# Optimization experiments

Measured on AMD Instinct MI355X. Metric: run time of the kernel, lower is better.

The kernel has to match this reference:

```python
import jax, jax.numpy as jnp
import numpy as np

B, T, D, H, HS = 4, 1024, 1024, 16, 64
DW, DA, DG, DV = 64, 64, 128, 32
DM = H * HS  # == D here
EPS = 1e-5
DECAY_C = -0.606531  # -exp(-0.5)


def setup_inputs() -> dict:
    key = jax.random.key(0)
    ks = jax.random.split(key, 24)
    n = lambda k, s: jax.random.normal(k, s, dtype=jnp.float32)
    w = lambda k, s: n(k, s) * (1.0 / np.sqrt(s[0]))
    return dict(
        current=n(ks[0], (B, T, D)),
        prev=n(ks[1], (B, T, D)),
        v_first=n(ks[2], (B, T, DM)),
        rwkvag=jax.random.uniform(ks[3], (6, D), dtype=jnp.float32),
        rw_W=w(ks[4], (D, D)),
        w1=w(ks[5], (D, DW)), w2=w(ks[6], (DW, DM)), w2_b=n(ks[7], (DM,)) * 0.1,
        kw_W=w(ks[8], (D, DM)), vw_W=w(ks[9], (D, DM)),
        a1=w(ks[10], (D, DA)), a2=w(ks[11], (DA, DM)), a2_b=n(ks[12], (DM,)) * 0.1,
        v1=w(ks[13], (D, DV)), v2=w(ks[14], (DV, DM)), v2_b=n(ks[15], (DM,)) * 0.1,
        g1=w(ks[16], (D, DG)), g2=w(ks[17], (DG, DM)), g2_b=n(ks[18], (DM,)) * 0.1,
        k_k=jnp.ones((DM,)), k_a=jax.random.uniform(ks[19], (DM,), dtype=jnp.float32),
        r_k=jnp.ones((DM,)),
        gn_scale=jnp.ones((DM,)), gn_bias=jnp.zeros((DM,)),
        out_W=w(ks[20], (DM, D)),
    )


def _add_heads(x):
    return x.reshape(x.shape[:-1] + (H, HS))


def reference(current, prev, v_first, rwkvag, rw_W, w1, w2, w2_b, kw_W, vw_W,
              a1, a2, a2_b, v1, v2, v2_b, g1, g2, g2_b,
              k_k, k_a, r_k, gn_scale, gn_bias, out_W):
    diff = prev - current
    # per-channel token-shift mixing for the 6 branches: (B,T,6,D)
    x6 = current[..., None, :] + rwkvag * diff[..., None, :]
    xr, xw, xk, xv, xa, xg = (x6[..., i, :] for i in range(6))

    r = xr @ rw_W
    wl = jnp.tanh(xw @ w1) @ w2 + w2_b          # w-LoRA (tanh, bias_post)
    k = xk @ kw_W
    v = xv @ vw_W
    a = jax.nn.sigmoid((xa @ a1) @ a2 + a2_b)   # a-LoRA (bias_post) + sigmoid
    g = jax.nn.sigmoid(xg @ g1) @ g2 + g2_b     # g-LoRA (sigmoid act)

    kk = _add_heads(k * k_k)
    kk = kk / jnp.linalg.norm(kk, axis=-1, keepdims=True)
    k = k * (1.0 + (a - 1.0) * k_a)
    v = v + (v_first - v) * jax.nn.sigmoid((xv @ v1) @ v2 + v2_b)
    wdec = jnp.exp(DECAY_C * jax.nn.sigmoid(wl))  # decay in (exp(-0.6065), 1)

    rk_sum = _add_heads(r * k * r_k).sum(-1, keepdims=True)  # (B,T,H,1)
    rh, wh, kh, vh = _add_heads(r), _add_heads(wdec), _add_heads(k), _add_heads(v)
    at = -kk
    bt = kk * _add_heads(a)

    def step(state, xs):
        rt, wt, ktt, vt, att, btt = xs  # each (B,H,HS)
        sa = jnp.einsum('bhvk,bhk->bhv', state, att)
        state = (state * wt[:, :, None, :]
                 + sa[..., None] * btt[:, :, None, :]
                 + vt[..., None] * ktt[:, :, None, :])
        y = jnp.einsum('bhvk,bhk->bhv', state, rt)
        return state, y

    xs = tuple(jnp.moveaxis(x, 1, 0) for x in (rh, wh, kh, vh, at, bt))
    state0 = jnp.zeros((B, H, HS, HS), dtype=current.dtype)
    state, ys = jax.lax.scan(step, state0, xs)
    out = jnp.moveaxis(ys, 0, 1)  # (B,T,H,HS)

    # GroupNorm with n_head groups (normalize within each head)
    mu = out.mean(-1, keepdims=True)
    var = out.var(-1, keepdims=True)
    outn = (out - mu) * jax.lax.rsqrt(var + EPS)
    outn = outn.reshape(B, T, DM) * gn_scale + gn_bias

    outn = outn + (rk_sum * vh).reshape(B, T, DM)
    y = (outn * g) @ out_W
    return y, state, v_first
```

## Files before the change

kernel.cpp:

```cpp
#include <hip/hip_runtime.h>
#include <math.h>

#define NT 4096
#define DD 1024
#define NH 16
#define HSZ 64
#define GN_EPS 1e-5f
#define DECAY_C -0.606531f

typedef __attribute__((ext_vector_type(8))) short short8;
typedef __attribute__((ext_vector_type(4))) float float4v;

#define GLB(p) ((const __attribute__((address_space(1))) void*)(p))
#define LDS(p) ((__attribute__((address_space(3))) void*)(p))

__device__ __forceinline__ float sigm(float x) { return 1.f / (1.f + __expf(-x)); }

__device__ __forceinline__ unsigned short f2bf(float f) {
    unsigned int u = __float_as_uint(f);
    u = (u + 0x7fffu + ((u >> 16) & 1u)) >> 16;
    return (unsigned short)u;
}
__device__ __forceinline__ float bf2f(unsigned short h) {
    return __uint_as_float(((unsigned int)h) << 16);
}

__device__ __forceinline__ float row_sum16(float x) {
    int t;
    t = __builtin_amdgcn_update_dpp(0, __float_as_int(x), 0x128, 0xF, 0xF, true);
    x += __int_as_float(t);
    t = __builtin_amdgcn_update_dpp(0, __float_as_int(x), 0x124, 0xF, 0xF, true);
    x += __int_as_float(t);
    t = __builtin_amdgcn_update_dpp(0, __float_as_int(x), 0x122, 0xF, 0xF, true);
    x += __int_as_float(t);
    t = __builtin_amdgcn_update_dpp(0, __float_as_int(x), 0x121, 0xF, 0xF, true);
    x += __int_as_float(t);
    return x;
}

__global__ __launch_bounds__(256)
void mix6(const float* __restrict__ cur, const float* __restrict__ prev,
          const float* __restrict__ lam,
          ushort* __restrict__ xrh, ushort* __restrict__ xrl,
          ushort* __restrict__ xwh, ushort* __restrict__ xwl,
          ushort* __restrict__ xkh, ushort* __restrict__ xkl,
          ushort* __restrict__ xvh, ushort* __restrict__ xvl,
          ushort* __restrict__ xah, ushort* __restrict__ xal,
          ushort* __restrict__ xgh, ushort* __restrict__ xgl)
{
    const int tok = blockIdx.x;
    const int d0 = threadIdx.x * 4;
    const size_t base = (size_t)tok * DD + d0;
    float4 c = *(const float4*)(cur + base);
    float4 p = *(const float4*)(prev + base);
    float dx = p.x - c.x, dy = p.y - c.y, dz = p.z - c.z, dw = p.w - c.w;
    ushort* hs[6] = {xrh, xwh, xkh, xvh, xah, xgh};
    ushort* ls[6] = {xrl, xwl, xkl, xvl, xal, xgl};
#pragma unroll
    for (int j = 0; j < 6; j++) {
        float4 l = *(const float4*)(lam + j * DD + d0);
        float m0 = c.x + l.x * dx;
        float m1 = c.y + l.y * dy;
        float m2 = c.z + l.z * dz;
        float m3 = c.w + l.w * dw;
        ushort4 h;
        h.x = f2bf(m0); h.y = f2bf(m1); h.z = f2bf(m2); h.w = f2bf(m3);
        *(ushort4*)(hs[j] + base) = h;
        ushort4 lo;
        lo.x = f2bf(m0 - bf2f(h.x));
        lo.y = f2bf(m1 - bf2f(h.y));
        lo.z = f2bf(m2 - bf2f(h.z));
        lo.w = f2bf(m3 - bf2f(h.w));
        *(ushort4*)(ls[j] + base) = lo;
    }
}

__global__ __launch_bounds__(256)
void transpose_pad(const float* __restrict__ W, ushort* __restrict__ Wh,
                   ushort* __restrict__ Wl, int K, int N)
{
    __shared__ float tile[32][33];
    const int bx = blockIdx.x * 32;
    const int by = blockIdx.y * 32;
    const int tx = threadIdx.x, ty = threadIdx.y;
#pragma unroll
    for (int i = 0; i < 32; i += 8) {
        float v = 0.f;
        if (bx + tx < N) v = W[(size_t)(by + ty + i) * N + bx + tx];
        tile[ty + i][tx] = v;
    }
    __syncthreads();
#pragma unroll
    for (int i = 0; i < 32; i += 8) {
        float v = tile[tx][ty + i];
        ushort h = f2bf(v);
        size_t o = (size_t)(bx + ty + i) * K + by + tx;
        Wh[o] = h;
        if (Wl) Wl[o] = f2bf(v - bf2f(h));
    }
}

__global__ __launch_bounds__(256)
void gemm_mega1(const ushort* __restrict__ xrh, const ushort* __restrict__ xrl,
                const ushort* __restrict__ xwh, const ushort* __restrict__ xwl,
                const ushort* __restrict__ xkh, const ushort* __restrict__ xkl,
                const ushort* __restrict__ xvh, const ushort* __restrict__ xvl,
                const ushort* __restrict__ xah, const ushort* __restrict__ xal,
                const ushort* __restrict__ xgh, const ushort* __restrict__ xgl,
                const ushort* __restrict__ Bth, const ushort* __restrict__ Btl,
                float* __restrict__ r_buf, float* __restrict__ k_buf,
                float* __restrict__ v_buf,
                ushort* __restrict__ hwh, ushort* __restrict__ hwl,
                ushort* __restrict__ hah, ushort* __restrict__ hal,
                ushort* __restrict__ hvh, ushort* __restrict__ hvl,
                ushort* __restrict__ hgh, ushort* __restrict__ hgl)
{
    __shared__ ushort AsH[128 * 32];
    __shared__ ushort BsH[128 * 32];
    __shared__ ushort AsL[128 * 32];
    __shared__ ushort BsL[128 * 32];
    const int cb = blockIdx.y;
    const ushort* Ah; const ushort* Al;
    if (cb < 8)       { Ah = xrh; Al = xrl; }
    else if (cb < 16) { Ah = xkh; Al = xkl; }
    else if (cb < 24) { Ah = xvh; Al = xvl; }
    else if (cb == 24){ Ah = xwh; Al = xwl; }
    else if (cb == 25){ Ah = xah; Al = xal; }
    else if (cb == 26){ Ah = xvh; Al = xvl; }
    else              { Ah = xgh; Al = xgl; }

    const int tid = threadIdx.x;
    const int rowBase = blockIdx.x * 128;
    const int colBase = cb * 128;
    const int lane = tid & 63;
    const int wave = tid >> 6;
    const int wm = wave >> 1, wn = wave & 1;
    const int m15 = lane & 15, quad = lane >> 4;

    float4v zero4 = {0.f, 0.f, 0.f, 0.f};
    float4v acc[4][4];
#pragma unroll
    for (int i = 0; i < 4; i++)
#pragma unroll
        for (int j = 0; j < 4; j++) acc[i][j] = zero4;

    for (int k0 = 0; k0 < 1024; k0 += 32) {
#pragma unroll
        for (int i = 0; i < 2; i++) {
            int idx = i * 256 + tid;
            int r = idx >> 2, seg = idx & 3;
            size_t aoff = (size_t)(rowBase + r) * 1024 + k0 + seg * 8;
            size_t boff = (size_t)(colBase + r) * 1024 + k0 + seg * 8;
            int dst = (i * 256 + (tid & ~63)) * 8;
            __builtin_amdgcn_global_load_lds(GLB(Ah + aoff), LDS(AsH + dst), 16, 0, 0);
            __builtin_amdgcn_global_load_lds(GLB(Bth + boff), LDS(BsH + dst), 16, 0, 0);
            __builtin_amdgcn_global_load_lds(GLB(Al + aoff), LDS(AsL + dst), 16, 0, 0);
            __builtin_amdgcn_global_load_lds(GLB(Btl + boff), LDS(BsL + dst), 16, 0, 0);
        }
        __syncthreads();
        short8 ah[4], bh[4], al[4], bl[4];
#pragma unroll
        for (int mi = 0; mi < 4; mi++) {
            ah[mi] = *(const short8*)(AsH + (wm * 64 + mi * 16 + m15) * 32 + quad * 8);
            al[mi] = *(const short8*)(AsL + (wm * 64 + mi * 16 + m15) * 32 + quad * 8);
        }
#pragma unroll
        for (int ni = 0; ni < 4; ni++) {
            bh[ni] = *(const short8*)(BsH + (wn * 64 + ni * 16 + m15) * 32 + quad * 8);
            bl[ni] = *(const short8*)(BsL + (wn * 64 + ni * 16 + m15) * 32 + quad * 8);
        }
#pragma unroll
        for (int mi = 0; mi < 4; mi++)
#pragma unroll
            for (int ni = 0; ni < 4; ni++) {
                acc[mi][ni] = __builtin_amdgcn_mfma_f32_16x16x32_bf16(al[mi], bh[ni], acc[mi][ni], 0, 0, 0);
                acc[mi][ni] = __builtin_amdgcn_mfma_f32_16x16x32_bf16(ah[mi], bl[ni], acc[mi][ni], 0, 0, 0);
                acc[mi][ni] = __builtin_amdgcn_mfma_f32_16x16x32_bf16(ah[mi], bh[ni], acc[mi][ni], 0, 0, 0);
            }
        __syncthreads();
    }

#pragma unroll
    for (int mi = 0; mi < 4; mi++) {
#pragma unroll
        for (int ni = 0; ni < 4; ni++) {
            int c = wn * 64 + ni * 16 + m15;
#pragma unroll
            for (int rr = 0; rr < 4; rr++) {
                int row = rowBase + wm * 64 + mi * 16 + quad * 4 + rr;
                float v = acc[mi][ni][rr];
                if (cb < 24) {
                    float* dst = (cb < 8) ? r_buf : (cb < 16) ? k_buf : v_buf;
                    int n = (cb & 7) * 128 + c;
                    dst[(size_t)row * 1024 + n] = v;
                } else if (cb == 24) {
                    if (c < 64) {
                        float t = tanhf(v);
                        ushort h = f2bf(t);
                        hwh[(size_t)row * 64 + c] = h;
                        hwl[(size_t)row * 64 + c] = f2bf(t - bf2f(h));
                    }
                } else if (cb == 25) {
                    if (c < 64) {
                        ushort h = f2bf(v);
                        hah[(size_t)row * 64 + c] = h;
                        hal[(size_t)row * 64 + c] = f2bf(v - bf2f(h));
                    }
                } else if (cb == 26) {
                    if (c < 32) {
                        ushort h = f2bf(v);
                        hvh[(size_t)row * 32 + c] = h;
                        hvl[(size_t)row * 32 + c] = f2bf(v - bf2f(h));
                    }
                } else {
                    float t = sigm(v);
                    ushort h = f2bf(t);
                    hgh[(size_t)row * 128 + c] = h;
                    hgl[(size_t)row * 128 + c] = f2bf(t - bf2f(h));
                }
            }
        }
    }
}

__global__ __launch_bounds__(256)
void gemm_mega2(const ushort* __restrict__ hwh, const ushort* __restrict__ hwl,
                const ushort* __restrict__ hah, const ushort* __restrict__ hal,
                const ushort* __restrict__ hvh, const ushort* __restrict__ hvl,
                const ushort* __restrict__ hgh, const ushort* __restrict__ hgl,
                const ushort* __restrict__ w2Th, const ushort* __restrict__ w2Tl,
                const ushort* __restrict__ a2Th, const ushort* __restrict__ a2Tl,
                const ushort* __restrict__ v2Th, const ushort* __restrict__ v2Tl,
                const ushort* __restrict__ g2Th, const ushort* __restrict__ g2Tl,
                const float* __restrict__ w2_b, const float* __restrict__ a2_b,
                const float* __restrict__ v2_b, const float* __restrict__ g2_b,
                float* __restrict__ w_buf, float* __restrict__ a_buf,
                float* __restrict__ vg_buf, float* __restrict__ g_buf)
{
    __shared__ ushort AsH[128 * 32];
    __shared__ ushort BsH[128 * 32];
    __shared__ ushort AsL[128 * 32];
    __shared__ ushort BsL[128 * 32];
    const int cb = blockIdx.y;
    const int seg = cb >> 3;
    const int K = (seg == 2) ? 32 : (seg == 3) ? 128 : 64;
    const ushort *Ah, *Al, *Bh, *Bl;
    const float* bias;
    float* outp;
    if (seg == 0) { Ah = hwh; Al = hwl; Bh = w2Th; Bl = w2Tl; bias = w2_b; outp = w_buf; }
    else if (seg == 1) { Ah = hah; Al = hal; Bh = a2Th; Bl = a2Tl; bias = a2_b; outp = a_buf; }
    else if (seg == 2) { Ah = hvh; Al = hvl; Bh = v2Th; Bl = v2Tl; bias = v2_b; outp = vg_buf; }
    else { Ah = hgh; Al = hgl; Bh = g2Th; Bl = g2Tl; bias = g2_b; outp = g_buf; }

    const int tid = threadIdx.x;
    const int rowBase = blockIdx.x * 128;
    const int colBase = (cb & 7) * 128;
    const int lane = tid & 63;
    const int wave = tid >> 6;
    const int wm = wave >> 1, wn = wave & 1;
    const int m15 = lane & 15, quad = lane >> 4;

    float4v zero4 = {0.f, 0.f, 0.f, 0.f};
    float4v acc[4][4];
#pragma unroll
    for (int i = 0; i < 4; i++)
#pragma unroll
        for (int j = 0; j < 4; j++) acc[i][j] = zero4;

    for (int k0 = 0; k0 < K; k0 += 32) {
#pragma unroll
        for (int i = 0; i < 2; i++) {
            int idx = i * 256 + tid;
            int r = idx >> 2, s8 = idx & 3;
            size_t aoff = (size_t)(rowBase + r) * K + k0 + s8 * 8;
            size_t boff = (size_t)(colBase + r) * K + k0 + s8 * 8;
            int dst = (i * 256 + (tid & ~63)) * 8;
            __builtin_amdgcn_global_load_lds(GLB(Ah + aoff), LDS(AsH + dst), 16, 0, 0);
            __builtin_amdgcn_global_load_lds(GLB(Bh + boff), LDS(BsH + dst), 16, 0, 0);
            __builtin_amdgcn_global_load_lds(GLB(Al + aoff), LDS(AsL + dst), 16, 0, 0);
            __builtin_amdgcn_global_load_lds(GLB(Bl + boff), LDS(BsL + dst), 16, 0, 0);
        }
        __syncthreads();
        short8 ah[4], bh[4], al[4], bl[4];
#pragma unroll
        for (int mi = 0; mi < 4; mi++) {
            ah[mi] = *(const short8*)(AsH + (wm * 64 + mi * 16 + m15) * 32 + quad * 8);
            al[mi] = *(const short8*)(AsL + (wm * 64 + mi * 16 + m15) * 32 + quad * 8);
        }
#pragma unroll
        for (int ni = 0; ni < 4; ni++) {
            bh[ni] = *(const short8*)(BsH + (wn * 64 + ni * 16 + m15) * 32 + quad * 8);
            bl[ni] = *(const short8*)(BsL + (wn * 64 + ni * 16 + m15) * 32 + quad * 8);
        }
#pragma unroll
        for (int mi = 0; mi < 4; mi++)
#pragma unroll
            for (int ni = 0; ni < 4; ni++) {
                acc[mi][ni] = __builtin_amdgcn_mfma_f32_16x16x32_bf16(al[mi], bh[ni], acc[mi][ni], 0, 0, 0);
                acc[mi][ni] = __builtin_amdgcn_mfma_f32_16x16x32_bf16(ah[mi], bl[ni], acc[mi][ni], 0, 0, 0);
                acc[mi][ni] = __builtin_amdgcn_mfma_f32_16x16x32_bf16(ah[mi], bh[ni], acc[mi][ni], 0, 0, 0);
            }
        __syncthreads();
    }

#pragma unroll
    for (int mi = 0; mi < 4; mi++) {
#pragma unroll
        for (int ni = 0; ni < 4; ni++) {
            int col = colBase + wn * 64 + ni * 16 + m15;
            float bv = bias[col];
#pragma unroll
            for (int rr = 0; rr < 4; rr++) {
                int row = rowBase + wm * 64 + mi * 16 + quad * 4 + rr;
                float v = acc[mi][ni][rr] + bv;
                if (seg == 1 || seg == 2) v = sigm(v);
                outp[(size_t)row * 1024 + col] = v;
            }
        }
    }
}

__global__ __launch_bounds__(256)
void gemm_bf16s(const ushort* __restrict__ Ah, const ushort* __restrict__ Bh,
                float* __restrict__ outF, int N, int K)
{
    __shared__ ushort AsH[128 * 32];
    __shared__ ushort BsH[128 * 32];
    const int tid = threadIdx.x;
    const int rowBase = blockIdx.x * 128;
    const int colBase = blockIdx.y * 128;
    const int lane = tid & 63;
    const int wave = tid >> 6;
    const int wm = wave >> 1, wn = wave & 1;
    const int m15 = lane & 15, quad = lane >> 4;

    float4v zero4 = {0.f, 0.f, 0.f, 0.f};
    float4v acc[4][4];
#pragma unroll
    for (int i = 0; i < 4; i++)
#pragma unroll
        for (int j = 0; j < 4; j++) acc[i][j] = zero4;

    for (int k0 = 0; k0 < K; k0 += 32) {
#pragma unroll
        for (int i = 0; i < 2; i++) {
            int idx = i * 256 + tid;
            int r = idx >> 2, seg = idx & 3;
            size_t aoff = (size_t)(rowBase + r) * K + k0 + seg * 8;
            size_t boff = (size_t)(colBase + r) * K + k0 + seg * 8;
            int dst = (i * 256 + (tid & ~63)) * 8;
            __builtin_amdgcn_global_load_lds(GLB(Ah + aoff), LDS(AsH + dst), 16, 0, 0);
            __builtin_amdgcn_global_load_lds(GLB(Bh + boff), LDS(BsH + dst), 16, 0, 0);
        }
        __syncthreads();
        short8 ah[4], bh[4];
#pragma unroll
        for (int mi = 0; mi < 4; mi++)
            ah[mi] = *(const short8*)(AsH + (wm * 64 + mi * 16 + m15) * 32 + quad * 8);
#pragma unroll
        for (int ni = 0; ni < 4; ni++)
            bh[ni] = *(const short8*)(BsH + (wn * 64 + ni * 16 + m15) * 32 + quad * 8);
#pragma unroll
        for (int mi = 0; mi < 4; mi++)
#pragma unroll
            for (int ni = 0; ni < 4; ni++)
                acc[mi][ni] = __builtin_amdgcn_mfma_f32_16x16x32_bf16(ah[mi], bh[ni], acc[mi][ni], 0, 0, 0);
        __syncthreads();
    }

#pragma unroll
    for (int mi = 0; mi < 4; mi++) {
#pragma unroll
        for (int ni = 0; ni < 4; ni++) {
            int col = colBase + wn * 64 + ni * 16 + m15;
#pragma unroll
            for (int rr = 0; rr < 4; rr++) {
                int row = rowBase + wm * 64 + mi * 16 + quad * 4 + rr;
                outF[(size_t)row * N + col] = acc[mi][ni][rr];
            }
        }
    }
}

__global__ __launch_bounds__(256)
void elemwise1(const float* __restrict__ r_buf, float* __restrict__ wl_buf,
               float* __restrict__ k_buf, float* __restrict__ v_buf,
               float* __restrict__ kkn_buf, const float* __restrict__ a_buf,
               const float* __restrict__ vg_buf, const float* __restrict__ vfirst,
               const float* __restrict__ kkw, const float* __restrict__ kaw,
               const float* __restrict__ rkw, float* __restrict__ rk_sum)
{
    const int tok = blockIdx.x;
    const int tid = threadIdx.x;
    const int d0 = tid * 4;
    const size_t base = (size_t)tok * DD + d0;

    float4 k0 = *(const float4*)(k_buf + base);
    float4 a4 = *(const float4*)(a_buf + base);
    float4 wl = *(const float4*)(wl_buf + base);
    float4 v0 = *(const float4*)(v_buf + base);
    float4 vg = *(const float4*)(vg_buf + base);
    float4 vf = *(const float4*)(vfirst + base);
    float4 r4 = *(const float4*)(r_buf + base);
    float4 kkc = *(const float4*)(kkw + d0);
    float4 kac = *(const float4*)(kaw + d0);
    float4 rkc = *(const float4*)(rkw + d0);

    float kk0 = k0.x * kkc.x, kk1 = k0.y * kkc.y, kk2 = k0.z * kkc.z, kk3 = k0.w * kkc.w;
    float ss = kk0 * kk0 + kk1 * kk1 + kk2 * kk2 + kk3 * kk3;
    ss += __shfl_xor(ss, 1); ss += __shfl_xor(ss, 2);
    ss += __shfl_xor(ss, 4); ss += __shfl_xor(ss, 8);
    float rn = rsqrtf(ss);
    float4 kkn = { kk0 * rn, kk1 * rn, kk2 * rn, kk3 * rn };
    *(float4*)(kkn_buf + base) = kkn;

    float4 kf;
    kf.x = k0.x * (1.f + (a4.x - 1.f) * kac.x);
    kf.y = k0.y * (1.f + (a4.y - 1.f) * kac.y);
    kf.z = k0.z * (1.f + (a4.z - 1.f) * kac.z);
    kf.w = k0.w * (1.f + (a4.w - 1.f) * kac.w);
    *(float4*)(k_buf + base) = kf;

    float rk = r4.x * kf.x * rkc.x + r4.y * kf.y * rkc.y + r4.z * kf.z * rkc.z + r4.w * kf.w * rkc.w;
    rk += __shfl_xor(rk, 1); rk += __shfl_xor(rk, 2);
    rk += __shfl_xor(rk, 4); rk += __shfl_xor(rk, 8);
    if ((tid & 15) == 0) rk_sum[(size_t)tok * NH + (tid >> 4)] = rk;

    float4 vfin;
    vfin.x = v0.x + (vf.x - v0.x) * vg.x;
    vfin.y = v0.y + (vf.y - v0.y) * vg.y;
    vfin.z = v0.z + (vf.z - v0.z) * vg.z;
    vfin.w = v0.w + (vf.w - v0.w) * vg.w;
    *(float4*)(v_buf + base) = vfin;

    float4 wd;
    wd.x = __expf(DECAY_C * sigm(wl.x));
    wd.y = __expf(DECAY_C * sigm(wl.y));
    wd.z = __expf(DECAY_C * sigm(wl.z));
    wd.w = __expf(DECAY_C * sigm(wl.w));
    *(float4*)(wl_buf + base) = wd;
}

__global__ __launch_bounds__(256)
void scan_kernel(const float* __restrict__ r_buf, const float* __restrict__ w_buf,
                 const float* __restrict__ k_buf, const float* __restrict__ kkn_buf,
                 const float* __restrict__ a_buf, const float* __restrict__ v_buf,
                 float* __restrict__ out_scan, float* __restrict__ state_out)
{
    __shared__ float vec[16][5][64];
    __shared__ float vbuf[16][16];
    __shared__ float ybuf[16][16];
    const int bh = blockIdx.x;
    const int rg = blockIdx.y;
    const int b = bh >> 4, h = bh & 15;
    const int tid = threadIdx.x;
    const int row = tid >> 4, l16 = tid & 15;
    const int rowbase = rg * 16;
    const size_t tok0 = ((size_t)b * 1024) * DD + h * HSZ;
    float s0 = 0.f, s1 = 0.f, s2 = 0.f, s3 = 0.f;

    const int tld = tid >> 4;
    const int lld = (tid & 15) * 4;
    const int ft = tid >> 2, fl = (tid & 3) * 4;

    for (int c = 0; c < 64; c++) {
        if (c > 0 && tid < 64) {
            float4 yv = *(float4*)&ybuf[ft][fl];
            *(float4*)(out_scan + tok0 + (size_t)((c - 1) * 16 + ft) * DD + rowbase + fl) = yv;
        }
#pragma unroll
        for (int j = 0; j < 5; j++) {
            const float* bs = (j == 0) ? r_buf : (j == 1) ? w_buf : (j == 2) ? k_buf
                              : (j == 3) ? kkn_buf : a_buf;
            *(float4*)&vec[tld][j][lld] =
                *(const float4*)(bs + tok0 + (size_t)(c * 16 + tld) * DD + lld);
        }
        if (tid < 64) {
            *(float4*)&vbuf[ft][fl] =
                *(const float4*)(v_buf + tok0 + (size_t)(c * 16 + ft) * DD + rowbase + fl);
        }
        __syncthreads();

        for (int t = 0; t < 16; t++) {
            const float* vp = &vec[t][0][0];
            float4 r4 = *(const float4*)(vp + l16 * 4);
            float4 w4 = *(const float4*)(vp + 64 + l16 * 4);
            float4 k4 = *(const float4*)(vp + 128 + l16 * 4);
            float4 q4 = *(const float4*)(vp + 192 + l16 * 4);
            float4 a4 = *(const float4*)(vp + 256 + l16 * 4);
            float vv = vbuf[t][row];

            float sa = s0 * q4.x + s1 * q4.y + s2 * q4.z + s3 * q4.w;
            sa = row_sum16(sa);
            sa = -sa;

            s0 = s0 * w4.x + sa * (q4.x * a4.x) + vv * k4.x;
            s1 = s1 * w4.y + sa * (q4.y * a4.y) + vv * k4.y;
            s2 = s2 * w4.z + sa * (q4.z * a4.z) + vv * k4.z;
            s3 = s3 * w4.w + sa * (q4.w * a4.w) + vv * k4.w;

            float y = s0 * r4.x + s1 * r4.y + s2 * r4.z + s3 * r4.w;
            y = row_sum16(y);
            if (l16 == 0) ybuf[t][row] = y;
        }
        __syncthreads();
    }

    if (tid < 64) {
        float4 yv = *(float4*)&ybuf[ft][fl];
        *(float4*)(out_scan + tok0 + (size_t)(1008 + ft) * DD + rowbase + fl) = yv;
    }

    float* so = state_out + ((size_t)(b * NH + h) * HSZ + rowbase + row) * HSZ + l16 * 4;
    float4 sv = {s0, s1, s2, s3};
    *(float4*)so = sv;
}

__global__ __launch_bounds__(256)
void elemwise2(const float* __restrict__ out_scan, const float* __restrict__ rk_sum,
               const float* __restrict__ v_buf, const float* __restrict__ g_buf,
               const float* __restrict__ gscale, const float* __restrict__ gbias,
               ushort* __restrict__ z_buf)
{
    const int tok = blockIdx.x;
    const int tid = threadIdx.x;
    const int d0 = tid * 4;
    const size_t base = (size_t)tok * DD + d0;

    float4 o = *(const float4*)(out_scan + base);
    float sm = o.x + o.y + o.z + o.w;
    float ss = o.x * o.x + o.y * o.y + o.z * o.z + o.w * o.w;
    sm += __shfl_xor(sm, 1); sm += __shfl_xor(sm, 2);
    sm += __shfl_xor(sm, 4); sm += __shfl_xor(sm, 8);
    ss += __shfl_xor(ss, 1); ss += __shfl_xor(ss, 2);
    ss += __shfl_xor(ss, 4); ss += __shfl_xor(ss, 8);
    float mu = sm * (1.f / 64.f);
    float var = ss * (1.f / 64.f) - mu * mu;
    float rs = rsqrtf(var + GN_EPS);
    float rk = rk_sum[(size_t)tok * NH + (tid >> 4)];

    float4 v4 = *(const float4*)(v_buf + base);
    float4 g4 = *(const float4*)(g_buf + base);
    float4 gs = *(const float4*)(gscale + d0);
    float4 gb = *(const float4*)(gbias + d0);
    ushort4 z;
    z.x = f2bf(((o.x - mu) * rs * gs.x + gb.x + rk * v4.x) * g4.x);
    z.y = f2bf(((o.y - mu) * rs * gs.y + gb.y + rk * v4.y) * g4.y);
    z.z = f2bf(((o.z - mu) * rs * gs.z + gb.z + rk * v4.z) * g4.z);
    z.w = f2bf(((o.w - mu) * rs * gs.w + gb.w + rk * v4.w) * g4.w);
    *(ushort4*)(z_buf + base) = z;
}

extern "C" void kernel_launch(void* const* d_in, const int* in_sizes, int n_in,
                              void* d_out, int out_size, void* d_ws, size_t ws_size,
                              hipStream_t stream) {
    const float* cur    = (const float*)d_in[0];
    const float* prev   = (const float*)d_in[1];
    const float* vfirst = (const float*)d_in[2];
    const float* rwkvag = (const float*)d_in[3];
    const float* rw_W   = (const float*)d_in[4];
    const float* w1     = (const float*)d_in[5];
    const float* w2     = (const float*)d_in[6];
    const float* w2_b   = (const float*)d_in[7];
    const float* kw_W   = (const float*)d_in[8];
    const float* vw_W   = (const float*)d_in[9];
    const float* a1     = (const float*)d_in[10];
    const float* a2     = (const float*)d_in[11];
    const float* a2_b   = (const float*)d_in[12];
    const float* v1     = (const float*)d_in[13];
    const float* v2     = (const float*)d_in[14];
    const float* v2_b   = (const float*)d_in[15];
    const float* g1     = (const float*)d_in[16];
    const float* g2     = (const float*)d_in[17];
    const float* g2_b   = (const float*)d_in[18];
    const float* k_k    = (const float*)d_in[19];
    const float* k_a    = (const float*)d_in[20];
    const float* r_k    = (const float*)d_in[21];
    const float* gn_s   = (const float*)d_in[22];
    const float* gn_b   = (const float*)d_in[23];
    const float* out_W  = (const float*)d_in[24];

    float* out = (float*)d_out;
    float* y_out = out;
    float* state_out = out + (size_t)NT * DD;
    float* vf_out = state_out + (size_t)4 * NH * HSZ * HSZ;

    float* p = (float*)d_ws;
    const size_t big = (size_t)NT * DD;
    const size_t half = big / 2;
    float* r_buf = p;   p += big;
    float* k_buf = p;   p += big;
    float* v_buf = p;   p += big;
    float* xreg = p;
    ushort* xrh = (ushort*)(xreg);            ushort* xrl = (ushort*)(xreg + half);
    ushort* xwh = (ushort*)(xreg + 2*half);   ushort* xwl = (ushort*)(xreg + 3*half);
    ushort* xkh = (ushort*)(xreg + 4*half);   ushort* xkl = (ushort*)(xreg + 5*half);
    ushort* xvh = (ushort*)(xreg + 6*half);   ushort* xvl = (ushort*)(xreg + 7*half);
    ushort* xah = (ushort*)(xreg + 8*half);   ushort* xal = (ushort*)(xreg + 9*half);
    ushort* xgh = (ushort*)(xreg + 10*half);  ushort* xgl = (ushort*)(xreg + 11*half);
    p += 12 * half;
    float* w_buf   = xreg + 0 * half;
    float* a_buf   = xreg + 2 * half;
    float* vg_buf  = xreg + 4 * half;
    float* os_buf  = vg_buf;
    float* g_buf   = xreg + 6 * half;
    float* kkn_buf = xreg + 8 * half;
    float* btreg = p;
    ushort* Bth = (ushort*)btreg;
    ushort* Btl = (ushort*)(btreg + 1835008);
    p += 2 * 1835008;
    ushort* z_bf  = (ushort*)btreg;
    ushort* outTh = (ushort*)(btreg + 2097152);
    ushort* w2Th = (ushort*)p; p += 32768; ushort* w2Tl = (ushort*)p; p += 32768;
    ushort* a2Th = (ushort*)p; p += 32768; ushort* a2Tl = (ushort*)p; p += 32768;
    ushort* v2Th = (ushort*)p; p += 16384; ushort* v2Tl = (ushort*)p; p += 16384;
    ushort* g2Th = (ushort*)p; p += 65536; ushort* g2Tl = (ushort*)p; p += 65536;
    ushort* hwh = (ushort*)p; p += 131072; ushort* hwl = (ushort*)p; p += 131072;
    ushort* hah = (ushort*)p; p += 131072; ushort* hal = (ushort*)p; p += 131072;
    ushort* hvh = (ushort*)p; p += 65536;  ushort* hvl = (ushort*)p; p += 65536;
    ushort* hgh = (ushort*)p; p += 262144; ushort* hgl = (ushort*)p; p += 262144;
    float* rks_buf = p;        p += 65536;

    dim3 blk(256);
    dim3 t32x8(32, 8);

    transpose_pad<<<dim3(32, 32), t32x8, 0, stream>>>(rw_W, Bth + (size_t)0 * 1024,    Btl + (size_t)0 * 1024,    1024, 1024);
    transpose_pad<<<dim3(32, 32), t32x8, 0, stream>>>(kw_W, Bth + (size_t)1024 * 1024, Btl + (size_t)1024 * 1024, 1024, 1024);
    transpose_pad<<<dim3(32, 32), t32x8, 0, stream>>>(vw_W, Bth + (size_t)2048 * 1024, Btl + (size_t)2048 * 1024, 1024, 1024);
    transpose_pad<<<dim3(4, 32), t32x8, 0, stream>>>(w1, Bth + (size_t)3072 * 1024, Btl + (size_t)3072 * 1024, 1024, 64);
    transpose_pad<<<dim3(4, 32), t32x8, 0, stream>>>(a1, Bth + (size_t)3200 * 1024, Btl + (size_t)3200 * 1024, 1024, 64);
    transpose_pad<<<dim3(4, 32), t32x8, 0, stream>>>(v1, Bth + (size_t)3328 * 1024, Btl + (size_t)3328 * 1024, 1024, 32);
    transpose_pad<<<dim3(4, 32), t32x8, 0, stream>>>(g1, Bth + (size_t)3456 * 1024, Btl + (size_t)3456 * 1024, 1024, 128);
    transpose_pad<<<dim3(32, 2), t32x8, 0, stream>>>(w2, w2Th, w2Tl, 64, 1024);
    transpose_pad<<<dim3(32, 2), t32x8, 0, stream>>>(a2, a2Th, a2Tl, 64, 1024);
    transpose_pad<<<dim3(32, 1), t32x8, 0, stream>>>(v2, v2Th, v2Tl, 32, 1024);
    transpose_pad<<<dim3(32, 4), t32x8, 0, stream>>>(g2, g2Th, g2Tl, 128, 1024);

    mix6<<<NT, blk, 0, stream>>>(cur, prev, rwkvag,
                                 xrh, xrl, xwh, xwl, xkh, xkl,
                                 xvh, xvl, xah, xal, xgh, xgl);

    gemm_mega1<<<dim3(32, 28), blk, 0, stream>>>(
        xrh, xrl, xwh, xwl, xkh, xkl, xvh, xvl, xah, xal, xgh, xgl,
        Bth, Btl, r_buf, k_buf, v_buf,
        hwh, hwl, hah, hal, hvh, hvl, hgh, hgl);

    transpose_pad<<<dim3(32, 32), t32x8, 0, stream>>>(out_W, outTh, nullptr, 1024, 1024);

    gemm_mega2<<<dim3(32, 32), blk, 0, stream>>>(
        hwh, hwl, hah, hal, hvh, hvl, hgh, hgl,
        w2Th, w2Tl, a2Th, a2Tl, v2Th, v2Tl, g2Th, g2Tl,
        w2_b, a2_b, v2_b, g2_b,
        w_buf, a_buf, vg_buf, g_buf);

    elemwise1<<<NT, blk, 0, stream>>>(r_buf, w_buf, k_buf, v_buf, kkn_buf, a_buf,
                                      vg_buf, vfirst, k_k, k_a, r_k, rks_buf);

    scan_kernel<<<dim3(64, 4), blk, 0, stream>>>(r_buf, w_buf, k_buf, kkn_buf, a_buf, v_buf,
                                                 os_buf, state_out);

    elemwise2<<<NT, blk, 0, stream>>>(os_buf, rks_buf, v_buf, g_buf, gn_s, gn_b, z_bf);

    gemm_bf16s<<<dim3(32, 8), blk, 0, stream>>>(z_bf, outTh, y_out, 1024, 1024);

    hipMemcpyAsync(vf_out, vfirst, (size_t)NT * DD * sizeof(float),
                   hipMemcpyDeviceToDevice, stream);
}
```

Before: 612.8 us.

## Double-buffer scan inputs via async global-to-LDS loads and defer y reduction

Reworks the recurrent scan kernel so the next chunk of r/w/k/kk/a/v is prefetched asynchronously into a second LDS buffer with global_load_lds while the current chunk is processed. The per-step y cross-lane reduction is removed from the serial chain: partial dot products go to LDS and are summed once per chunk by all threads. Token loads are software-pipelined in register pairs. The aim is to hide global memory latency and shorten the dependent per-step critical path, at the cost of more LDS usage and reliance on async-load completion ordering with a single barrier per chunk.

Measured after the change: 541.6 us. 11.6% less time.

```diff
diff --git a/kernel.cpp b/kernel.cpp
--- a/kernel.cpp
+++ b/kernel.cpp
@@ -447,69 +447,102 @@
                  const float* __restrict__ a_buf, const float* __restrict__ v_buf,
                  float* __restrict__ out_scan, float* __restrict__ state_out)
 {
-    __shared__ float vec[16][5][64];
-    __shared__ float vbuf[16][16];
-    __shared__ float ybuf[16][16];
+    __shared__ float vecJ[2][5][16][64];
+    __shared__ float vbuf2[2][16][16];
+    __shared__ float ypart[2][16][16][16];
     const int bh = blockIdx.x;
     const int rg = blockIdx.y;
     const int b = bh >> 4, h = bh & 15;
     const int tid = threadIdx.x;
     const int row = tid >> 4, l16 = tid & 15;
+    const int lofs = l16 * 4;
     const int rowbase = rg * 16;
     const size_t tok0 = ((size_t)b * 1024) * DD + h * HSZ;
     float s0 = 0.f, s1 = 0.f, s2 = 0.f, s3 = 0.f;
 
-    const int tld = tid >> 4;
-    const int lld = (tid & 15) * 4;
-    const int ft = tid >> 2, fl = (tid & 3) * 4;
+#define STAGE(cc, bb) do {                                                        \
+    const int tt_ = tid >> 4;                                                     \
+    const int dd4_ = (tid & 15) * 4;                                              \
+    size_t gofs_ = tok0 + (size_t)((cc) * 16 + tt_) * DD + dd4_;                  \
+    float* db_ = &vecJ[bb][0][0][0] + ((tid >> 6) << 8);                          \
+    __builtin_amdgcn_global_load_lds(GLB(r_buf + gofs_),   LDS(db_),        16, 0, 0); \
+    __builtin_amdgcn_global_load_lds(GLB(w_buf + gofs_),   LDS(db_ + 1024), 16, 0, 0); \
+    __builtin_amdgcn_global_load_lds(GLB(k_buf + gofs_),   LDS(db_ + 2048), 16, 0, 0); \
+    __builtin_amdgcn_global_load_lds(GLB(kkn_buf + gofs_), LDS(db_ + 3072), 16, 0, 0); \
+    __builtin_amdgcn_global_load_lds(GLB(a_buf + gofs_),   LDS(db_ + 4096), 16, 0, 0); \
+    if (tid < 64) {                                                               \
+        size_t vofs_ = tok0 + (size_t)((cc) * 16 + (tid >> 2)) * DD + rowbase + (tid & 3) * 4; \
+        __builtin_amdgcn_global_load_lds(GLB(v_buf + vofs_), LDS(&vbuf2[bb][0][0]), 16, 0, 0); \
+    }                                                                             \
+} while (0)
+
+#define LD_TOK(P, tt) do {                                                        \
+    P##r = *(const float4*)(vb + (tt) * 64 + lofs);                               \
+    P##w = *(const float4*)(vb + 1024 + (tt) * 64 + lofs);                        \
+    P##k = *(const float4*)(vb + 2048 + (tt) * 64 + lofs);                        \
+    P##q = *(const float4*)(vb + 3072 + (tt) * 64 + lofs);                        \
+    P##a = *(const float4*)(vb + 4096 + (tt) * 64 + lofs);                        \
+    P##v = vbp[(tt) * 16 + row];                                                  \
+} while (0)
+
+#define STEP(P, tt) do {                                                          \
+    float sa_ = P##q.x * s0;                                                      \
+    sa_ = fmaf(P##q.y, s1, sa_);                                                  \
+    sa_ = fmaf(P##q.z, s2, sa_);                                                  \
+    sa_ = fmaf(P##q.w, s3, sa_);                                                  \
+    sa_ = row_sum16(sa_);                                                         \
+    float n0_ = P##q.x * P##a.x, n1_ = P##q.y * P##a.y;                           \
+    float n2_ = P##q.z * P##a.z, n3_ = P##q.w * P##a.w;                           \
+    float b0_ = fmaf(s0, P##w.x, P##v * P##k.x);                                  \
+    float b1_ = fmaf(s1, P##w.y, P##v * P##k.y);                                  \
+    float b2_ = fmaf(s2, P##w.z, P##v * P##k.z);                                  \
+    float b3_ = fmaf(s3, P##w.w, P##v * P##k.w);                                  \
+    s0 = fmaf(sa_, -n0_, b0_);                                                    \
+    s1 = fmaf(sa_, -n1_, b1_);                                                    \
+    s2 = fmaf(sa_, -n2_, b2_);                                                    \
+    s3 = fmaf(sa_, -n3_, b3_);                                                    \
+    float yp_ = P##r.x * s0;                                                      \
+    yp_ = fmaf(P##r.y, s1, yp_);                                                  \
+    yp_ = fmaf(P##r.z, s2, yp_);                                                  \
+    yp_ = fmaf(P##r.w, s3, yp_);                                                  \
+    ypart[buf][tt][row][l16] = yp_;                                               \
+} while (0)
+
+    STAGE(0, 0);
+    __syncthreads();
 
     for (int c = 0; c < 64; c++) {
-        if (c > 0 && tid < 64) {
-            float4 yv = *(float4*)&ybuf[ft][fl];
-            *(float4*)(out_scan + tok0 + (size_t)((c - 1) * 16 + ft) * DD + rowbase + fl) = yv;
-        }
-#pragma unroll
-        for (int j = 0; j < 5; j++) {
-            const float* bs = (j == 0) ? r_buf : (j == 1) ? w_buf : (j == 2) ? k_buf
-                              : (j == 3) ? kkn_buf : a_buf;
-            *(float4*)&vec[tld][j][lld] =
-                *(const float4*)(bs + tok0 + (size_t)(c * 16 + tld) * DD + lld);
-        }
-        if (tid < 64) {
-            *(float4*)&vbuf[ft][fl] =
-                *(const float4*)(v_buf + tok0 + (size_t)(c * 16 + ft) * DD + rowbase + fl);
+        const int buf = c & 1;
+        if (c < 63) STAGE(c + 1, buf ^ 1);
+        const float* vb  = &vecJ[buf][0][0][0];
+        const float* vbp = &vbuf2[buf][0][0];
+        float4 Ar, Aw, Ak, Aq, Aa; float Av;
+        float4 Br, Bw, Bk, Bq, Ba; float Bv;
+        LD_TOK(A, 0);
+#pragma unroll
+        for (int tp = 0; tp < 8; tp++) {
+            LD_TOK(B, 2 * tp + 1);
+            STEP(A, 2 * tp);
+            if (tp < 7) LD_TOK(A, 2 * tp + 2);
+            STEP(B, 2 * tp + 1);
         }
         __syncthreads();
-
-        for (int t = 0; t < 16; t++) {
-            const float* vp = &vec[t][0][0];
-            float4 r4 = *(const float4*)(vp + l16 * 4);
-            float4 w4 = *(const float4*)(vp + 64 + l16 * 4);
-            float4 k4 = *(const float4*)(vp + 128 + l16 * 4);
-            float4 q4 = *(const float4*)(vp + 192 + l16 * 4);
-            float4 a4 = *(const float4*)(vp + 256 + l16 * 4);
-            float vv = vbuf[t][row];
-
-            float sa = s0 * q4.x + s1 * q4.y + s2 * q4.z + s3 * q4.w;
-            sa = row_sum16(sa);
-            sa = -sa;
-
-            s0 = s0 * w4.x + sa * (q4.x * a4.x) + vv * k4.x;
-            s1 = s1 * w4.y + sa * (q4.y * a4.y) + vv * k4.y;
-            s2 = s2 * w4.z + sa * (q4.z * a4.z) + vv * k4.z;
-            s3 = s3 * w4.w + sa * (q4.w * a4.w) + vv * k4.w;
-
-            float y = s0 * r4.x + s1 * r4.y + s2 * r4.z + s3 * r4.w;
-            y = row_sum16(y);
-            if (l16 == 0) ybuf[t][row] = y;
-        }
-        __syncthreads();
-    }
-
-    if (tid < 64) {
-        float4 yv = *(float4*)&ybuf[ft][fl];
-        *(float4*)(out_scan + tok0 + (size_t)(1008 + ft) * DD + rowbase + fl) = yv;
-    }
+        {
+            const int t_ = tid >> 4, r_ = tid & 15;
+            const float* yp = &ypart[buf][t_][r_][0];
+            float4 y0 = *(const float4*)(yp);
+            float4 y1 = *(const float4*)(yp + 4);
+            float4 y2 = *(const float4*)(yp + 8);
+            float4 y3 = *(const float4*)(yp + 12);
+            float ys = ((y0.x + y0.y) + (y0.z + y0.w)) + ((y1.x + y1.y) + (y1.z + y1.w))
+                     + ((y2.x + y2.y) + (y2.z + y2.w)) + ((y3.x + y3.y) + (y3.z + y3.w));
+            out_scan[tok0 + (size_t)(c * 16 + t_) * DD + rowbase + r_] = ys;
+        }
+    }
+
+#undef STAGE
+#undef LD_TOK
+#undef STEP
 
     float* so = state_out + ((size_t)(b * NH + h) * HSZ + rowbase + row) * HSZ + l16 * 4;
     float4 sv = {s0, s1, s2, s3};
```
